# Optimization experiments

Hardware: AMD Instinct MI355X
Metric: run time of the kernel (lower is better)

Reference implementation:

```python
import jax, jax.numpy as jnp
import numpy as np

B = 64
SIZES = [5023, 1256, 314, 79, 20]
NV = [s + 1 for s in SIZES]          # vertex counts incl. padding vertex
K = 12                               # spiral length (all levels)
LAT = 128
ENC_F = [3, 16, 32, 64, 128]
DEC_IN = [128, 64, 32, 32, 16]
DEC_OUT = [64, 32, 32, 16, 3]


def setup_inputs() -> dict:
    keys = iter(jax.random.split(jax.random.key(0), 80))

    def nrm(shape, scale=1.0):
        return jax.random.normal(next(keys), shape, jnp.float32) * scale

    inp = {}
    inp['x_talking'] = nrm((B, NV[0], 3))
    inp['template'] = nrm((B, NV[0], 3))
    for i in range(4):
        inp['D%d' % i] = nrm((NV[i + 1], NV[i]), 1.0 / np.sqrt(NV[i]))
        inp['U%d' % i] = nrm((NV[i], NV[i + 1]), 1.0 / np.sqrt(NV[i + 1]))
    for i in range(4):
        fan = ENC_F[i] * K
        inp['enc_w%d' % i] = nrm((ENC_F[i + 1], fan), 1.0 / np.sqrt(fan))
        inp['enc_b%d' % i] = jnp.zeros((ENC_F[i + 1],), jnp.float32)
    inp['fc_enc_w'] = nrm((LAT, NV[4] * DEC_IN[0]), 1.0 / np.sqrt(NV[4] * DEC_IN[0]))
    inp['fc_enc_b'] = jnp.zeros((LAT,), jnp.float32)
    inp['fc_dec_w'] = nrm((NV[4] * DEC_IN[0], 2 * LAT), 1.0 / np.sqrt(2 * LAT))
    inp['fc_dec_b'] = jnp.zeros((NV[4] * DEC_IN[0],), jnp.float32)
    for i in range(5):
        fan = DEC_IN[i] * K
        inp['dec_w%d' % i] = nrm((DEC_OUT[i], fan), 1.0 / np.sqrt(fan))
        inp['dec_b%d' % i] = jnp.zeros((DEC_OUT[i],), jnp.float32)
    for i in range(4):
        inp['S%d' % i] = jax.random.randint(next(keys), (NV[i], K), 0, NV[i], jnp.int32)
    return inp


def _spiral_conv(x, S, W, b, act):
    # x: [B, N, F]; S: [N, K] spiral neighbor indices; W: [out, K*F] (torch Linear layout)
    Bv, Nv, F = x.shape
    g = x[:, S, :].reshape(Bv, Nv, K * F)            # spiral neighbor gather
    y = act(jnp.einsum('bnf,of->bno', g, W) + b)     # gather-GEMM + activation
    mask = jnp.ones((1, Nv, 1), y.dtype).at[0, -1, 0].set(0.0)  # zero out padding vertex
    return y * mask


def _forward(x_talking, template, D, U, enc, fc_enc_w, fc_enc_b, fc_dec_w, fc_dec_b, dec, S):
    elu = jax.nn.elu
    # encode_talking
    x = x_talking
    for i in range(4):
        x = _spiral_conv(x, S[i], enc[i][0], enc[i][1], elu)
        x = jnp.einsum('mn,bnf->bmf', D[i], x)       # downsample
    z = x.reshape(B, -1) @ fc_enc_w.T + fc_enc_b     # [B, latent]
    # decode(z, z)
    h = jnp.concatenate([z, z], axis=1) @ fc_dec_w.T + fc_dec_b
    x = h.reshape(B, NV[4], DEC_IN[0])
    for i in range(3):
        x = jnp.einsum('mn,bnf->bmf', U[3 - i], x)   # upsample
        x = _spiral_conv(x, S[3 - i], dec[i][0], dec[i][1], elu)
    x = jnp.einsum('mn,bnf->bmf', U[0], x)
    x = _spiral_conv(x, S[0], dec[3][0], dec[3][1], elu)
    x = _spiral_conv(x, S[0], dec[4][0], dec[4][1], lambda v: v)  # identity activation
    return x, x + template


def reference(x_talking, template, D0, D1, D2, D3, U0, U1, U2, U3,
              enc_w0, enc_b0, enc_w1, enc_b1, enc_w2, enc_b2, enc_w3, enc_b3,
              fc_enc_w, fc_enc_b, fc_dec_w, fc_dec_b,
              dec_w0, dec_b0, dec_w1, dec_b1, dec_w2, dec_b2, dec_w3, dec_b3, dec_w4, dec_b4,
              S0, S1, S2, S3):
    return _forward(
        x_talking, template,
        [D0, D1, D2, D3], [U0, U1, U2, U3],
        [(enc_w0, enc_b0), (enc_w1, enc_b1), (enc_w2, enc_b2), (enc_w3, enc_b3)],
        fc_enc_w, fc_enc_b, fc_dec_w, fc_dec_b,
        [(dec_w0, dec_b0), (dec_w1, dec_b1), (dec_w2, dec_b2), (dec_w3, dec_b3), (dec_w4, dec_b4)],
        [S0, S1, S2, S3])
```

## Files before the change

kernel.cpp:

```cpp
#include <hip/hip_runtime.h>
#include <cstddef>


#define BATCH 64
#define SPK 12

typedef __attribute__((ext_vector_type(8))) short bf16x8;
typedef __attribute__((ext_vector_type(4))) short bf16x4;
typedef __attribute__((ext_vector_type(4))) float f32x4;

__device__ __forceinline__ unsigned short f2bf(float x) {
    union { float f; unsigned int u; } v; v.f = x;
    unsigned int r = v.u + 0x7FFF + ((v.u >> 16) & 1);
    return (unsigned short)(r >> 16);
}

__global__ __launch_bounds__(256) void f32_to_bf16_kernel(
    const float* __restrict__ in, unsigned short* __restrict__ out, int n8)
{
    int i = blockIdx.x * 256 + threadIdx.x;
    if (i < n8) {
        const float* p = in + (size_t)i * 8;
        bf16x8 r;
#pragma unroll
        for (int j = 0; j < 8; ++j) r[j] = (short)f2bf(p[j]);
        *(bf16x8*)(out + (size_t)i * 8) = r;
    }
}

__global__ __launch_bounds__(256) void a_bf16_pad_kernel(
    const float* __restrict__ A, unsigned short* __restrict__ Ap,
    int M, int K, int Kp, int total)
{
    int i = blockIdx.x * 256 + threadIdx.x;
    if (i >= total) return;
    int kp8 = Kp >> 3;
    int m = i / kp8;
    int k0 = (i - m * kp8) * 8;
    bf16x8 r;
    if (m < M) {
        const float* src = A + (size_t)m * K + k0;
#pragma unroll
        for (int j = 0; j < 8; ++j) {
            float v = (k0 + j < K) ? src[j] : 0.f;
            r[j] = (short)f2bf(v);
        }
    } else {
#pragma unroll
        for (int j = 0; j < 8; ++j) r[j] = 0;
    }
    *(bf16x8*)(Ap + (size_t)m * Kp + k0) = r;
}

__global__ __launch_bounds__(256) void w_frag16_kernel(
    const unsigned short* __restrict__ Wb, unsigned short* __restrict__ Wfs,
    int KF, int total)
{
    int i = blockIdx.x * 256 + threadIdx.x;
    if (i >= total) return;
    int j    = i & 7;
    int lane = (i >> 3) & 63;
    int s    = i >> 9;
    int l15  = lane & 15;
    int quad = (lane >> 4) & 3;
    Wfs[i] = Wb[l15 * KF + s * 32 + quad * 8 + j];
}

template<int LOGF, int OBF16>
__global__ __launch_bounds__(64, 4) void conv_cmfma_kernel(
    const unsigned short* __restrict__ x, const int* __restrict__ S,
    const unsigned short* __restrict__ Wfs, const float* __restrict__ bias,
    void* __restrict__ yv, int Nv, int elu_flag, int swz)
{
    constexpr int F     = 1 << LOGF;
    constexpr int KF    = SPK * F;
    constexpr int NS    = KF / 32;
    constexpr int RPADu = (LOGF == 5) ? 40 : 24;
    __shared__ unsigned short Gs[12 * 16 * RPADu];

    const int lane = threadIdx.x;
    const int l15  = lane & 15;
    const int quad = (lane >> 4) & 3;

    int bx = blockIdx.x, bz = blockIdx.z;
    if (swz) {
        const int gx = gridDim.x;
        const int total = gx * gridDim.z;
        int bid = bx + gx * bz;
        const int chunk = total >> 3;
        int sid = (bid & 7) * chunk + (bid >> 3);
        bx = sid % gx;
        bz = sid / gx;
    }
    const int n0 = bx * 16;
    const int b  = bz;
    const size_t xb = (size_t)b * Nv;

    int4 sv;
    {
        int g = lane >> 4; if (g > 2) g = 2;
        int n = n0 + l15; if (n >= Nv) n = 0;
        sv = *(const int4*)(S + n * SPK + g * 4);
    }

    if constexpr (LOGF == 5) {
        const int grow = lane >> 2, gchk = lane & 3;
#pragma unroll
        for (int k = 0; k < 12; ++k) {
            int sel = ((k >> 2) << 4) | grow;
            int comp = k & 3;
            int src = (comp == 0) ? __shfl(sv.x, sel)
                    : (comp == 1) ? __shfl(sv.y, sel)
                    : (comp == 2) ? __shfl(sv.z, sel)
                                  : __shfl(sv.w, sel);
            bf16x8 v = *(const bf16x8*)(x + ((xb + src) << 5) + gchk * 8);
            *(bf16x8*)&Gs[k * 16 * RPADu + grow * RPADu + gchk * 8] = v;
        }
    } else {
        const int khalf = lane >> 5, grow = (lane >> 1) & 15, gchk = lane & 1;
#pragma unroll
        for (int g = 0; g < 6; ++g) {
            int k0 = 2 * g;
            int sel0 = ((k0 >> 2) << 4) | grow;
            int sel1 = (((k0 + 1) >> 2) << 4) | grow;
            int s0 = ((k0 & 3) == 0) ? __shfl(sv.x, sel0) : __shfl(sv.z, sel0);
            int s1 = (((k0 + 1) & 3) == 1) ? __shfl(sv.y, sel1) : __shfl(sv.w, sel1);
            int src = khalf ? s1 : s0;
            int k   = k0 + khalf;
            bf16x8 v = *(const bf16x8*)(x + ((xb + src) << 4) + gchk * 8);
            *(bf16x8*)&Gs[k * 16 * RPADu + grow * RPADu + gchk * 8] = v;
        }
    }

    f32x4 acc0 = (f32x4){0.f, 0.f, 0.f, 0.f};
    f32x4 acc1 = (f32x4){0.f, 0.f, 0.f, 0.f};
#pragma unroll
    for (int s = 0; s < NS; ++s) {
        int kf = s * 32 + quad * 8;
        int k  = kf >> LOGF;
        int f  = kf & (F - 1);
        bf16x8 a = *(const bf16x8*)&Gs[k * 16 * RPADu + l15 * RPADu + f];
        bf16x8 w = *(const bf16x8*)(Wfs + (s * 64 + lane) * 8);
        if (s & 1) acc1 = __builtin_amdgcn_mfma_f32_16x16x32_bf16(a, w, acc1, 0, 0, 0);
        else       acc0 = __builtin_amdgcn_mfma_f32_16x16x32_bf16(a, w, acc0, 0, 0, 0);
    }

    float bv = bias[l15];
#pragma unroll
    for (int reg = 0; reg < 4; ++reg) {
        int nn = n0 + quad * 4 + reg;
        if (nn >= Nv) continue;
        float v = acc0[reg] + acc1[reg] + bv;
        if (elu_flag && v <= 0.f) v = expm1f(v);
        if (nn == Nv - 1) v = 0.f;
        size_t off = ((size_t)b * Nv + nn) * 16 + l15;
        if (OBF16) ((unsigned short*)yv)[off] = f2bf(v);
        else       ((float*)yv)[off] = v;
    }
}

template<int LOGF, int OBF16>
__global__ __launch_bounds__(64) void conv_wmfma_kernel(
    const unsigned short* __restrict__ x, const int* __restrict__ S,
    const unsigned short* __restrict__ Wb, const float* __restrict__ bias,
    void* __restrict__ yv, int Nv, int O, int elu_flag, int swz)
{
    constexpr int F  = 1 << LOGF;
    constexpr int KF = SPK * F;
    constexpr int NS = KF / 32;
    const int lane = threadIdx.x;
    const int l15  = lane & 15;
    const int quad = lane >> 4;

    int bx = blockIdx.x, by = blockIdx.y, bz = blockIdx.z;
    if (swz) {
        const int gx = gridDim.x, gy = gridDim.y;
        const int total = gx * gy * gridDim.z;
        int bid = bx + gx * (by + gy * bz);
        const int chunk = total >> 3;
        int sid = (bid & 7) * chunk + (bid >> 3);
        bx = sid % gx; sid /= gx;
        by = sid % gy;
        bz = sid / gy;
    }

    const int n0   = bx * 16;
    const int o    = by * 16 + l15;
    const int b    = bz;
    const size_t xb = (size_t)b * Nv;

    const int n  = n0 + l15;
    const int ng = (n < Nv) ? n : 0;
    const unsigned short* wrow = Wb + (size_t)o * KF;

    f32x4 acc0 = (f32x4){0.f, 0.f, 0.f, 0.f};
    f32x4 acc1 = (f32x4){0.f, 0.f, 0.f, 0.f};
#pragma unroll
    for (int s = 0; s < NS; ++s) {
        int kf  = s * 32 + quad * 8;
        int k   = kf >> LOGF;
        int f   = kf & (F - 1);
        int src = S[ng * SPK + k];
        bf16x8 a = *(const bf16x8*)(x + ((xb + src) << LOGF) + f);
        bf16x8 w = *(const bf16x8*)(wrow + kf);
        if (s & 1) acc1 = __builtin_amdgcn_mfma_f32_16x16x32_bf16(a, w, acc1, 0, 0, 0);
        else       acc0 = __builtin_amdgcn_mfma_f32_16x16x32_bf16(a, w, acc0, 0, 0, 0);
    }
    float bv = bias[o];
#pragma unroll
    for (int reg = 0; reg < 4; ++reg) {
        int nn = n0 + quad * 4 + reg;
        if (nn >= Nv) continue;
        float v = acc0[reg] + acc1[reg] + bv;
        if (elu_flag && v <= 0.f) v = expm1f(v);
        if (nn == Nv - 1) v = 0.f;
        size_t off = ((size_t)b * Nv + nn) * O + o;
        if (OBF16) ((unsigned short*)yv)[off] = f2bf(v);
        else       ((float*)yv)[off] = v;
    }
}

template<int LOGF>
__global__ __launch_bounds__(256) void conv_mfma32_kernel(
    const unsigned short* __restrict__ x, const int* __restrict__ S,
    const unsigned short* __restrict__ Wb, const float* __restrict__ bias,
    float* __restrict__ y, int Nv, int KF, int elu_flag)
{
    constexpr int PAD = 40;
    __shared__ unsigned short Gs[2][256 * PAD];

    const int b    = blockIdx.x;
    const int n0   = blockIdx.y * 256;
    const int tid  = threadIdx.x;
    const int lane = tid & 63;
    const int wave = tid >> 6;
    const int wm   = wave * 64;
    const int l15  = lane & 15;
    const int quad = lane >> 4;
    const size_t xb = (size_t)b * Nv;
    const int nslab = KF >> 5;

    f32x4 acc[4][2];
#pragma unroll
    for (int t = 0; t < 4; ++t)
#pragma unroll
        for (int o = 0; o < 2; ++o) acc[t][o] = (f32x4){0.f, 0.f, 0.f, 0.f};

    auto gath = [&](int k0, bf16x8* g) {
        int n = n0 + tid;
        if (n < Nv) {
#pragma unroll
            for (int j = 0; j < 4; ++j) {
                int kf  = k0 + j * 8;
                int k   = kf >> LOGF;
                int f   = kf & ((1 << LOGF) - 1);
                int src = S[n * SPK + k];
                g[j] = *(const bf16x8*)(x + ((xb + src) << LOGF) + f);
            }
        } else {
#pragma unroll
            for (int j = 0; j < 4; ++j)
#pragma unroll
                for (int e = 0; e < 8; ++e) g[j][e] = 0;
        }
    };
    auto put = [&](int buf, const bf16x8* g) {
#pragma unroll
        for (int j = 0; j < 4; ++j)
            *(bf16x8*)&Gs[buf][tid * PAD + j * 8] = g[j];
    };
    auto wfrag = [&](int k0, int o16) {
        return *(const bf16x8*)(Wb + (size_t)(o16 * 16 + l15) * KF + k0 + quad * 8);
    };

    bf16x8 gcur[4], gnext[4];
    gath(0, gcur);
    put(0, gcur);
    __syncthreads();

    for (int s = 0; s < nslab; ++s) {
        const int cur = s & 1;
        const bool more = (s + 1) < nslab;
        if (more) gath((s + 1) * 32, gnext);
        bf16x8 wf0 = wfrag(s * 32, 0);
        bf16x8 wf1 = wfrag(s * 32, 1);
#pragma unroll
        for (int t = 0; t < 4; ++t) {
            bf16x8 a = *(const bf16x8*)&Gs[cur][(wm + t * 16 + l15) * PAD + quad * 8];
            acc[t][0] = __builtin_amdgcn_mfma_f32_16x16x32_bf16(a, wf0, acc[t][0], 0, 0, 0);
            acc[t][1] = __builtin_amdgcn_mfma_f32_16x16x32_bf16(a, wf1, acc[t][1], 0, 0, 0);
        }
        if (more) {
            put(cur ^ 1, gnext);
            __syncthreads();
        }
    }

    float bv0 = bias[l15];
    float bv1 = bias[16 + l15];
#pragma unroll
    for (int t = 0; t < 4; ++t)
#pragma unroll
        for (int reg = 0; reg < 4; ++reg) {
            int n = n0 + wm + t * 16 + quad * 4 + reg;
            if (n >= Nv) continue;
            float v0 = acc[t][0][reg] + bv0;
            float v1 = acc[t][1][reg] + bv1;
            if (elu_flag) {
                if (v0 <= 0.f) v0 = expm1f(v0);
                if (v1 <= 0.f) v1 = expm1f(v1);
            }
            if (n == Nv - 1) { v0 = 0.f; v1 = 0.f; }
            size_t off = ((size_t)b * Nv + n) * 32 + l15;
            y[off]      = v0;
            y[off + 16] = v1;
        }
}

__global__ __launch_bounds__(256) void dsamp_mfma3_kernel(
    const unsigned short* __restrict__ Ab, const unsigned short* __restrict__ Xt,
    float* __restrict__ Y, int M, int Kp, int logF, int kchunk,
    int atomic_flag, int swz)
{
    constexpr int PAD = 40;
    __shared__ unsigned short As[2][128 * PAD];
    __shared__ unsigned short Bs[2][128 * PAD];

    int bx = blockIdx.x, by = blockIdx.y, bz = blockIdx.z;
    if (swz) {
        const int gx = gridDim.x, gy = gridDim.y;
        const int total = gx * gy * gridDim.z;
        int bid = bx + gx * (by + gy * bz);
        const int chunk = total >> 3;
        int sid = (bid & 7) * chunk + (bid >> 3);
        bx = sid % gx; sid /= gx;
        by = sid % gy;
        bz = sid / gy;
    }

    const int fmask = (1 << logF) - 1;
    const int m0   = bx * 128;
    const int c0   = by * 128;
    const int kbeg = bz * kchunk;
    int kend = kbeg + kchunk; if (kend > Kp) kend = Kp;
    const int nslab = (kend - kbeg + 31) >> 5;

    const int tid  = threadIdx.x;
    const int lane = tid & 63;
    const int wave = tid >> 6;
    const int wm   = (wave >> 1) * 64;
    const int wn   = (wave & 1) * 64;
    const int l15  = lane & 15;
    const int quad = lane >> 4;

    const int s_row = tid >> 2;
    const int s_k8  = (tid & 3) * 8;

    f32x4 acc[4][4];
#pragma unroll
    for (int i = 0; i < 4; ++i)
#pragma unroll
        for (int j = 0; j < 4; ++j) acc[i][j] = (f32x4){0.f, 0.f, 0.f, 0.f};

    bf16x8 apre[2], bpre[2];

    auto loadAB = [&](int ko) {
        apre[0] = *(const bf16x8*)(Ab + (size_t)(m0 + s_row)      * Kp + ko + s_k8);
        apre[1] = *(const bf16x8*)(Ab + (size_t)(m0 + s_row + 64) * Kp + ko + s_k8);
        bpre[0] = *(const bf16x8*)(Xt + (size_t)(c0 + s_row)      * Kp + ko + s_k8);
        bpre[1] = *(const bf16x8*)(Xt + (size_t)(c0 + s_row + 64) * Kp + ko + s_k8);
    };
    auto stage = [&](int buf) {
        *(bf16x8*)&As[buf][s_row * PAD + s_k8]        = apre[0];
        *(bf16x8*)&As[buf][(s_row + 64) * PAD + s_k8] = apre[1];
        *(bf16x8*)&Bs[buf][s_row * PAD + s_k8]        = bpre[0];
        *(bf16x8*)&Bs[buf][(s_row + 64) * PAD + s_k8] = bpre[1];
    };

    loadAB(kbeg);
    stage(0);
    __syncthreads();

    for (int s = 0; s < nslab; ++s) {
        const int cur = s & 1;
        const bool more = (s + 1) < nslab;
        if (more) loadAB(kbeg + (s + 1) * 32);

        bf16x8 af[4], bfr[4];
#pragma unroll
        for (int t = 0; t < 4; ++t) {
            af[t]  = *(const bf16x8*)&As[cur][(wm + t * 16 + l15) * PAD + quad * 8];
            bfr[t] = *(const bf16x8*)&Bs[cur][(wn + t * 16 + l15) * PAD + quad * 8];
        }
#pragma unroll
        for (int tm = 0; tm < 4; ++tm)
#pragma unroll
            for (int tn = 0; tn < 4; ++tn)
                acc[tm][tn] = __builtin_amdgcn_mfma_f32_16x16x32_bf16(af[tm], bfr[tn], acc[tm][tn], 0, 0, 0);

        if (more) { stage(cur ^ 1); __syncthreads(); }
    }

#pragma unroll
    for (int tm = 0; tm < 4; ++tm)
#pragma unroll
        for (int tn = 0; tn < 4; ++tn)
#pragma unroll
            for (int reg = 0; reg < 4; ++reg) {
                int m  = m0 + wm + tm * 16 + quad * 4 + reg;
                int cc = c0 + wn + tn * 16 + l15;
                if (m < M) {
                    int bb = cc >> logF, f = cc & fmask;
                    float* dst = Y + (((size_t)bb * M + m) << logF) + f;
                    if (atomic_flag) atomicAdd(dst, acc[tm][tn][reg]);
                    else *dst = acc[tm][tn][reg];
                }
            }
}

__global__ __launch_bounds__(256) void dsamp_mfma2_kernel(
    const unsigned short* __restrict__ Ap, const float* __restrict__ X,
    float* __restrict__ Y, int M, int K, int Kp, int logF, int kchunk,
    int atomic_flag)
{
    constexpr int PAD = 40;
    __shared__ unsigned short Xs[2][64 * PAD];

    const int fmask = (1 << logF) - 1;
    const int m0   = blockIdx.x * 64;
    const int c0   = blockIdx.y * 64;
    const int kbeg = blockIdx.z * kchunk;
    int kend = kbeg + kchunk; if (kend > K) kend = K;
    const int nslab = (kend - kbeg + 31) >> 5;

    const int tid  = threadIdx.x;
    const int lane = tid & 63;
    const int wave = tid >> 6;
    const int wm   = (wave >> 1) * 32;
    const int wn   = (wave & 1) * 32;
    const int l15  = lane & 15;
    const int quad = lane >> 4;

    const int skk  = tid >> 4;
    const int scg  = (tid & 15) * 4;
    const int cB   = c0 + scg;
    const int xbb  = cB >> logF;
    const int xf   = cB & fmask;
    const size_t xrowbase = (((size_t)xbb * K) << logF) + xf;

    const int mA0 = m0 + wm + l15;
    const int mA1 = mA0 + 16;
    const int kaoff = quad * 8;

    f32x4 acc[2][2];
    acc[0][0] = acc[0][1] = acc[1][0] = acc[1][1] = (f32x4){0.f, 0.f, 0.f, 0.f};

    float4 xn0, xn1;
    bf16x8 ac0, ac1, an0, an1;

    {
        int k = kbeg + skk;
        xn0 = make_float4(0.f, 0.f, 0.f, 0.f);
        if (k < kend) xn0 = *(const float4*)(X + xrowbase + ((size_t)k << logF));
        k = kbeg + 16 + skk;
        xn1 = make_float4(0.f, 0.f, 0.f, 0.f);
        if (k < kend) xn1 = *(const float4*)(X + xrowbase + ((size_t)k << logF));
        int ka = kbeg + kaoff;
        ac0 = *(const bf16x8*)(Ap + (size_t)mA0 * Kp + ka);
        ac1 = *(const bf16x8*)(Ap + (size_t)mA1 * Kp + ka);
        unsigned short* p = &Xs[0][0];
        p[(scg + 0) * PAD + skk] = f2bf(xn0.x);
        p[(scg + 1) * PAD + skk] = f2bf(xn0.y);
        p[(scg + 2) * PAD + skk] = f2bf(xn0.z);
        p[(scg + 3) * PAD + skk] = f2bf(xn0.w);
        int kk1 = 16 + skk;
        p[(scg + 0) * PAD + kk1] = f2bf(xn1.x);
        p[(scg + 1) * PAD + kk1] = f2bf(xn1.y);
        p[(scg + 2) * PAD + kk1] = f2bf(xn1.z);
        p[(scg + 3) * PAD + kk1] = f2bf(xn1.w);
    }
    __syncthreads();

    for (int s = 0; s < nslab; ++s) {
        const int cur = s & 1;
        const bool more = (s + 1 < nslab);
        if (more) {
            int k0 = kbeg + (s + 1) * 32;
            int k = k0 + skk;
            xn0 = make_float4(0.f, 0.f, 0.f, 0.f);
            if (k < kend) xn0 = *(const float4*)(X + xrowbase + ((size_t)k << logF));
            k = k0 + 16 + skk;
            xn1 = make_float4(0.f, 0.f, 0.f, 0.f);
            if (k < kend) xn1 = *(const float4*)(X + xrowbase + ((size_t)k << logF));
            int ka = k0 + kaoff;
            an0 = *(const bf16x8*)(Ap + (size_t)mA0 * Kp + ka);
            an1 = *(const bf16x8*)(Ap + (size_t)mA1 * Kp + ka);
        }
        {
            const unsigned short* p = &Xs[cur][0];
            bf16x8 b0 = *(const bf16x8*)&p[(wn +      l15) * PAD + quad * 8];
            bf16x8 b1 = *(const bf16x8*)&p[(wn + 16 + l15) * PAD + quad * 8];
            acc[0][0] = __builtin_amdgcn_mfma_f32_16x16x32_bf16(ac0, b0, acc[0][0], 0, 0, 0);
            acc[0][1] = __builtin_amdgcn_mfma_f32_16x16x32_bf16(ac0, b1, acc[0][1], 0, 0, 0);
            acc[1][0] = __builtin_amdgcn_mfma_f32_16x16x32_bf16(ac1, b0, acc[1][0], 0, 0, 0);
            acc[1][1] = __builtin_amdgcn_mfma_f32_16x16x32_bf16(ac1, b1, acc[1][1], 0, 0, 0);
        }
        if (more) {
            unsigned short* q = &Xs[cur ^ 1][0];
            q[(scg + 0) * PAD + skk] = f2bf(xn0.x);
            q[(scg + 1) * PAD + skk] = f2bf(xn0.y);
            q[(scg + 2) * PAD + skk] = f2bf(xn0.z);
            q[(scg + 3) * PAD + skk] = f2bf(xn0.w);
            int kk1 = 16 + skk;
            q[(scg + 0) * PAD + kk1] = f2bf(xn1.x);
            q[(scg + 1) * PAD + kk1] = f2bf(xn1.y);
            q[(scg + 2) * PAD + kk1] = f2bf(xn1.z);
            q[(scg + 3) * PAD + kk1] = f2bf(xn1.w);
            __syncthreads();
            ac0 = an0; ac1 = an1;
        }
    }

#pragma unroll
    for (int tm = 0; tm < 2; ++tm)
#pragma unroll
        for (int tn = 0; tn < 2; ++tn)
#pragma unroll
            for (int reg = 0; reg < 4; ++reg) {
                int m  = m0 + wm + tm * 16 + quad * 4 + reg;
                int cc = c0 + wn + tn * 16 + l15;
                if (m < M) {
                    int bb = cc >> logF, f = cc & fmask;
                    float* dst = Y + (((size_t)bb * M + m) << logF) + f;
                    if (atomic_flag) atomicAdd(dst, acc[tm][tn][reg]);
                    else *dst = acc[tm][tn][reg];
                }
            }
}

template<int MT, int OT>
__global__ __launch_bounds__(256) void conv_gemm_kernel(
    const float* __restrict__ x, const int* __restrict__ S,
    const float* __restrict__ W, const float* __restrict__ bias,
    float* __restrict__ y, int Nv, int logF, int O, int KF, int KFr,
    int elu_flag)
{
    constexpr int CT = OT / 4;
    constexpr int RT = 256 / CT;
    static_assert(RT * 4 == MT, "tile shape");
    __shared__ float Gs[32][MT];
    __shared__ float Ws[32][OT];

    const int b   = blockIdx.x;
    const int n0  = blockIdx.y * MT;
    const int tid = threadIdx.x;
    const int cx  = tid % CT;
    const int ry  = tid / CT;
    const int r0  = ry * 4;
    const int o0  = cx * 4;
    const int fmask = (1 << logF) - 1;
    const size_t xb = (size_t)b * Nv;

    float acc[4][4];
#pragma unroll
    for (int i = 0; i < 4; ++i)
#pragma unroll
        for (int j = 0; j < 4; ++j) acc[i][j] = 0.f;

    for (int k0 = 0; k0 < KF; k0 += 32) {
        constexpr int GSLOTS = MT * 8;
#pragma unroll
        for (int i = 0; i < GSLOTS / 256; ++i) {
            int idx = tid + i * 256;
            int r   = idx & (MT - 1);
            int jg  = idx / MT;
            int j0  = jg * 4;
            int n   = n0 + r;
            int kf  = k0 + j0;
            float4 v = make_float4(0.f, 0.f, 0.f, 0.f);
            if (n < Nv && kf < KFr) {
                int k   = kf >> logF;
                int f   = kf & fmask;
                int src = S[n * SPK + k];
                v = *(const float4*)(x + ((xb + src) << logF) + f);
            }
            Gs[j0 + 0][r] = v.x; Gs[j0 + 1][r] = v.y;
            Gs[j0 + 2][r] = v.z; Gs[j0 + 3][r] = v.w;
        }
        constexpr int WSLOTS = OT * 8;
#pragma unroll
        for (int i = 0; i < (WSLOTS + 255) / 256; ++i) {
            int idx = tid + i * 256;
            if (WSLOTS >= 256 || idx < WSLOTS) {
                int o  = idx & (OT - 1);
                int jg = idx / OT;
                int j0 = jg * 4;
                float4 v = *(const float4*)(W + (size_t)o * KF + k0 + j0);
                Ws[j0 + 0][o] = v.x; Ws[j0 + 1][o] = v.y;
                Ws[j0 + 2][o] = v.z; Ws[j0 + 3][o] = v.w;
            }
        }
        __syncthreads();
#pragma unroll
        for (int kk = 0; kk < 32; ++kk) {
            float4 g = *(const float4*)&Gs[kk][r0];
            float4 w = *(const float4*)&Ws[kk][o0];
            acc[0][0] += g.x * w.x; acc[0][1] += g.x * w.y; acc[0][2] += g.x * w.z; acc[0][3] += g.x * w.w;
            acc[1][0] += g.y * w.x; acc[1][1] += g.y * w.y; acc[1][2] += g.y * w.z; acc[1][3] += g.y * w.w;
            acc[2][0] += g.z * w.x; acc[2][1] += g.z * w.y; acc[2][2] += g.z * w.z; acc[2][3] += g.z * w.w;
            acc[3][0] += g.w * w.x; acc[3][1] += g.w * w.y; acc[3][2] += g.w * w.z; acc[3][3] += g.w * w.w;
        }
        __syncthreads();
    }

    float4 bv = *(const float4*)(bias + o0);
#pragma unroll
    for (int i = 0; i < 4; ++i) {
        int n = n0 + r0 + i;
        if (n >= Nv) continue;
        float v0 = acc[i][0] + bv.x;
        float v1 = acc[i][1] + bv.y;
        float v2 = acc[i][2] + bv.z;
        float v3 = acc[i][3] + bv.w;
        if (elu_flag) {
            v0 = v0 > 0.f ? v0 : expm1f(v0);
            v1 = v1 > 0.f ? v1 : expm1f(v1);
            v2 = v2 > 0.f ? v2 : expm1f(v2);
            v3 = v3 > 0.f ? v3 : expm1f(v3);
        }
        if (n == Nv - 1) { v0 = v1 = v2 = v3 = 0.f; }
        *(float4*)(y + ((size_t)b * Nv + n) * O + o0) = make_float4(v0, v1, v2, v3);
    }
}

template<int OBF16>
__global__ __launch_bounds__(256) void dsamp_kernel(
    const float* __restrict__ A, const float* __restrict__ X,
    void* __restrict__ Yv, int M, int N, int F)
{
    __shared__ float As[16][68];
    __shared__ float Xs[16][64];

    const int m0  = blockIdx.x * 64;
    const int c0  = blockIdx.y * 64;
    const int tid = threadIdx.x;
    const int tx  = tid & 15;
    const int ty  = tid >> 4;

    float acc[4][4];
#pragma unroll
    for (int i = 0; i < 4; ++i)
#pragma unroll
        for (int j = 0; j < 4; ++j) acc[i][j] = 0.f;

    for (int k0 = 0; k0 < N; k0 += 16) {
#pragma unroll
        for (int p = 0; p < 4; ++p) {
            int r  = (tid >> 4) + p * 16;
            int kk = tid & 15;
            int m  = m0 + r;
            int n  = k0 + kk;
            float v = 0.f;
            if (m < M && n < N) v = A[(size_t)m * N + n];
            As[kk][r] = v;
        }
        {
            int kk = tid >> 4;
            int cc = (tid & 15) * 4;
            int n  = k0 + kk;
            float4 v = make_float4(0.f, 0.f, 0.f, 0.f);
            if (n < N) {
                int c  = c0 + cc;
                int bb = c / F;
                int f  = c - bb * F;
                v = *(const float4*)(X + ((size_t)bb * N + n) * F + f);
            }
            *(float4*)&Xs[kk][cc] = v;
        }
        __syncthreads();
#pragma unroll
        for (int kk = 0; kk < 16; ++kk) {
            float4 av = *(const float4*)&As[kk][ty * 4];
            float4 xv = *(const float4*)&Xs[kk][tx * 4];
            acc[0][0] += av.x * xv.x; acc[0][1] += av.x * xv.y; acc[0][2] += av.x * xv.z; acc[0][3] += av.x * xv.w;
            acc[1][0] += av.y * xv.x; acc[1][1] += av.y * xv.y; acc[1][2] += av.y * xv.z; acc[1][3] += av.y * xv.w;
            acc[2][0] += av.z * xv.x; acc[2][1] += av.z * xv.y; acc[2][2] += av.z * xv.z; acc[2][3] += av.z * xv.w;
            acc[3][0] += av.w * xv.x; acc[3][1] += av.w * xv.y; acc[3][2] += av.w * xv.z; acc[3][3] += av.w * xv.w;
        }
        __syncthreads();
    }

    const int cbase = c0 + tx * 4;
    const int bb = cbase / F;
    const int f  = cbase - bb * F;
#pragma unroll
    for (int i = 0; i < 4; ++i) {
        int m = m0 + ty * 4 + i;
        if (m < M) {
            size_t off = ((size_t)bb * M + m) * F + f;
            if (OBF16) {
                bf16x4 v;
                v[0] = (short)f2bf(acc[i][0]); v[1] = (short)f2bf(acc[i][1]);
                v[2] = (short)f2bf(acc[i][2]); v[3] = (short)f2bf(acc[i][3]);
                *(bf16x4*)((unsigned short*)Yv + off) = v;
            } else {
                *(float4*)((float*)Yv + off) =
                    make_float4(acc[i][0], acc[i][1], acc[i][2], acc[i][3]);
            }
        }
    }
}

__global__ __launch_bounds__(256) void fc_wave_kernel(
    const float* __restrict__ in, const float* __restrict__ W,
    const float* __restrict__ bias, float* __restrict__ out,
    int In, int O, int dup)
{
    const int gw   = blockIdx.x * 4 + (threadIdx.x >> 6);
    const int lane = threadIdx.x & 63;
    const int b = gw / O;
    const int o = gw - b * O;
    const float* xr = in + (size_t)b * In;
    float acc = 0.f;
    if (dup) {
        const float* wr = W + (size_t)o * (2 * In);
        for (int k = lane; k < In; k += 64)
            acc += xr[k] * (wr[k] + wr[In + k]);
    } else {
        const float* wr = W + (size_t)o * In;
        for (int k = lane; k < In; k += 64)
            acc += xr[k] * wr[k];
    }
#pragma unroll
    for (int off = 32; off > 0; off >>= 1)
        acc += __shfl_down(acc, off, 64);
    if (lane == 0) out[(size_t)b * O + o] = acc + bias[o];
}

__global__ __launch_bounds__(256) void xpose_bf16_kernel(
    const float* __restrict__ x, unsigned short* __restrict__ xt,
    int K, int Kp, int logF)
{
    const int c  = blockIdx.y * 256 + threadIdx.x;
    const int k0 = blockIdx.x * 8;
    const int bb = c >> logF;
    const int f  = c & ((1 << logF) - 1);
    const float* src = x + (((size_t)bb * K) << logF) + f;
    bf16x8 r;
#pragma unroll
    for (int j = 0; j < 8; ++j) {
        int k = k0 + j;
        float v = (k < K) ? src[(size_t)k << logF] : 0.f;
        r[j] = (short)f2bf(v);
    }
    *(bf16x8*)(xt + (size_t)c * Kp + k0) = r;
}

__global__ __launch_bounds__(256) void pad_e0_w_kernel(
    const float* __restrict__ w, float* __restrict__ wp)
{
    int i = blockIdx.x * 256 + threadIdx.x;
    if (i < 1024) {
        int o = i >> 6, kf = i & 63;
        int k = kf >> 2, f = kf & 3;
        wp[i] = (f < 3 && k < 12) ? w[o * 36 + k * 3 + f] : 0.f;
    }
}
__global__ __launch_bounds__(256) void pad_x4_kernel(
    const float* __restrict__ x, float* __restrict__ xp, int n)
{
    int i = blockIdx.x * 256 + threadIdx.x;
    if (i < n) {
        int f = i & 3, nb = i >> 2;
        xp[i] = (f < 3) ? x[nb * 3 + f] : 0.f;
    }
}
__global__ __launch_bounds__(256) void pad_c4_w_kernel(
    const float* __restrict__ w, const float* __restrict__ b,
    float* __restrict__ wp, float* __restrict__ bp)
{
    int i = blockIdx.x * 256 + threadIdx.x;
    if (i < 3072) {
        int o = i / 192;
        wp[i] = (o < 3) ? w[i] : 0.f;
    }
    if (i < 16) bp[i] = (i < 3) ? b[i] : 0.f;
}
__global__ __launch_bounds__(256) void extract_add_kernel(
    const float* __restrict__ cp, const float* __restrict__ t,
    float* __restrict__ o0, float* __restrict__ o1, int n)
{
    int i = blockIdx.x * 256 + threadIdx.x;
    if (i < n) {
        int f = i % 3, nb = i / 3;
        float v = cp[(size_t)nb * 16 + f];
        o0[i] = v;
        o1[i] = v + t[i];
    }
}


static inline int ilog2(int v) { int l = 0; while ((1 << l) < v) ++l; return l; }

static inline void a_bf16_launch(const float* A, unsigned short* Ap, int M, int K,
                                 int Mp, int Kp, hipStream_t s)
{
    int total = Mp * (Kp >> 3);
    a_bf16_pad_kernel<<<(total + 255) / 256, 256, 0, s>>>(A, Ap, M, K, Kp, total);
}

static inline void dsamp_mfma2_launch(const unsigned short* Ap, const float* X,
                                      float* Y, int M, int K, int Kp, int F,
                                      int ks, hipStream_t s)
{
    int kchunk = (K + ks - 1) / ks;
    kchunk = (kchunk + 31) & ~31;
    int ksz = (K + kchunk - 1) / kchunk;
    dim3 grid((M + 63) / 64, F, ksz);
    dsamp_mfma2_kernel<<<grid, 256, 0, s>>>(Ap, X, Y, M, K, Kp, ilog2(F), kchunk,
                                            ksz > 1 ? 1 : 0);
}

static inline void dsamp_mfma3_launch(const unsigned short* Ab, const unsigned short* Xt,
                                      float* Y, int M, int Kp, int F,
                                      int ks, hipStream_t s)
{
    int slabs = Kp >> 5;
    int kchunk = ((slabs + ks - 1) / ks) * 32;
    int ksz = (Kp + kchunk - 1) / kchunk;
    int gx = (M + 127) / 128, gy = (BATCH * F) / 128;
    int total = gx * gy * ksz;
    int swz = (ksz > 1 && (total & 7) == 0) ? 1 : 0;
    dim3 grid(gx, gy, ksz);
    dsamp_mfma3_kernel<<<grid, 256, 0, s>>>(Ab, Xt, Y, M, Kp, ilog2(F), kchunk,
                                            ksz > 1 ? 1 : 0, swz);
}

template<int OBF16>
static inline void dsamp_launch(const float* A, const float* X, void* Y,
                                int M, int N, int F, hipStream_t s)
{
    dim3 grid((M + 63) / 64, F);
    dsamp_kernel<OBF16><<<grid, 256, 0, s>>>(A, X, Y, M, N, F);
}

extern "C" void kernel_launch(void* const* d_in, const int* in_sizes, int n_in,
                              void* d_out, int out_size, void* d_ws, size_t ws_size,
                              hipStream_t stream)
{
    const float* x_talking = (const float*)d_in[0];
    const float* templ     = (const float*)d_in[1];
    const float* D0 = (const float*)d_in[2];
    const float* U0 = (const float*)d_in[3];
    const float* D1 = (const float*)d_in[4];
    const float* U1 = (const float*)d_in[5];
    const float* D2 = (const float*)d_in[6];
    const float* U2 = (const float*)d_in[7];
    const float* D3 = (const float*)d_in[8];
    const float* U3 = (const float*)d_in[9];
    const float* enc_w0 = (const float*)d_in[10]; const float* enc_b0 = (const float*)d_in[11];
    const float* enc_w1 = (const float*)d_in[12]; const float* enc_b1 = (const float*)d_in[13];
    const float* enc_w2 = (const float*)d_in[14]; const float* enc_b2 = (const float*)d_in[15];
    const float* enc_w3 = (const float*)d_in[16]; const float* enc_b3 = (const float*)d_in[17];
    const float* fc_enc_w = (const float*)d_in[18]; const float* fc_enc_b = (const float*)d_in[19];
    const float* fc_dec_w = (const float*)d_in[20]; const float* fc_dec_b = (const float*)d_in[21];
    const float* dec_w0 = (const float*)d_in[22]; const float* dec_b0 = (const float*)d_in[23];
    const float* dec_w1 = (const float*)d_in[24]; const float* dec_b1 = (const float*)d_in[25];
    const float* dec_w2 = (const float*)d_in[26]; const float* dec_b2 = (const float*)d_in[27];
    const float* dec_w3 = (const float*)d_in[28]; const float* dec_b3 = (const float*)d_in[29];
    const float* dec_w4 = (const float*)d_in[30]; const float* dec_b4 = (const float*)d_in[31];
    const int* S0 = (const int*)d_in[32];
    const int* S1 = (const int*)d_in[33];
    const int* S2 = (const int*)d_in[34];
    const int* S3 = (const int*)d_in[35];

    float* bufA = (float*)d_ws;
    float* bufB = bufA + 10289152;

    float* out0 = (float*)d_out;
    float* out1 = out0 + 964608;

    unsigned short* Xt_e0 = (unsigned short*)(bufB + 1290240);
    unsigned short* Xt_c2 = (unsigned short*)bufB;
    unsigned short* U0b   = (unsigned short*)(bufB + 1400000);
    unsigned short* Wb_e2 = (unsigned short*)(bufB + 4700000);
    unsigned short* Wb_e3 = (unsigned short*)(bufB + 4715000);
    unsigned short* Wb_c0 = (unsigned short*)(bufB + 4765000);
    unsigned short* Wb_c1 = (unsigned short*)(bufB + 4815000);
    float* xpad   = bufA + 5200000;
    float* WpE0   = bufA + 6600000;
    unsigned short* D0b   = (unsigned short*)(bufA + 6700000);
    unsigned short* D1b   = (unsigned short*)(bufA + 9950000);
    unsigned short* U1b   = (unsigned short*)(bufA + 4000000);
    unsigned short* Wb_e1 = (unsigned short*)(bufA + 10160000);
    unsigned short* Wb_c2 = (unsigned short*)(bufA + 10170000);
    unsigned short* Xb_e1   = (unsigned short*)(bufA + 5200000);
    unsigned short* Xb_e2   = (unsigned short*)(bufA + 2000000);
    unsigned short* Xb_c2in = (unsigned short*)(bufA + 2600000);
    unsigned short* Xb_c3 = (unsigned short*)bufB;
    unsigned short* Xb_c4 = (unsigned short*)(bufA + 5200000);
    unsigned short* Wb_c3 = (unsigned short*)bufA;
    float* WpC4   = bufA + 10000;
    float* BpC4   = bufA + 13500;
    unsigned short* Wb_c4  = (unsigned short*)(bufA + 14000);
    unsigned short* Wfs_c3 = (unsigned short*)(bufA + 16000);
    unsigned short* Wfs_c4 = (unsigned short*)(bufA + 20000);

    hipMemsetAsync(bufB, 0, (size_t)1287168 * sizeof(float), stream);

    pad_e0_w_kernel<<<4, 256, 0, stream>>>(enc_w0, WpE0);
    pad_x4_kernel<<<5024, 256, 0, stream>>>(x_talking, xpad, 1286144);
    a_bf16_launch(D0, D0b, 1257, 5024, 1280, 5024, stream);
    a_bf16_launch(D1, D1b, 315, 1257, 320, 1280, stream);
    f32_to_bf16_kernel<<<3, 256, 0, stream>>>(enc_w1, Wb_e1, 768);
    f32_to_bf16_kernel<<<6, 256, 0, stream>>>(dec_w2, Wb_c2, 1536);
    f32_to_bf16_kernel<<<12, 256, 0, stream>>>(enc_w2, Wb_e2, 3072);
    f32_to_bf16_kernel<<<48, 256, 0, stream>>>(enc_w3, Wb_e3, 12288);
    f32_to_bf16_kernel<<<48, 256, 0, stream>>>(dec_w0, Wb_c0, 12288);
    f32_to_bf16_kernel<<<12, 256, 0, stream>>>(dec_w1, Wb_c1, 3072);

    {
        dim3 grid(BATCH, (5024 + 255) / 256);
        conv_gemm_kernel<256, 16><<<grid, 256, 0, stream>>>(
            xpad, S0, WpE0, enc_b0, bufA, 5024, 2, 16, 64, 48, 1);
    }
    xpose_bf16_kernel<<<dim3(628, 4), 256, 0, stream>>>(bufA, Xt_e0, 5024, 5024, 4);
    dsamp_mfma3_launch(D0b, Xt_e0, bufB, 1257, 5024, 16, 8, stream);
    f32_to_bf16_kernel<<<629, 256, 0, stream>>>(bufB, Xb_e1, 160896);
    a_bf16_launch(U0, U0b, 5024, 1257, 5120, 1280, stream);
    a_bf16_launch(U1, U1b, 1257, 315, 1280, 320, stream);
    {
        dim3 grid(BATCH, (1257 + 255) / 256);
        conv_mfma32_kernel<4><<<grid, 256, 0, stream>>>(
            Xb_e1, S1, Wb_e1, enc_b1, bufA, 1257, 192, 1);
    }
    hipMemsetAsync(bufB, 0, (size_t)645120 * sizeof(float), stream);
    dsamp_mfma2_launch(D1b, bufA, bufB, 315, 1257, 1280, 32, 8, stream);
    f32_to_bf16_kernel<<<315, 256, 0, stream>>>(bufB, Xb_e2, 80640);
    {
        dim3 grid((315 + 15) / 16, 64 / 16, BATCH);
        conv_wmfma_kernel<5, 0><<<grid, 64, 0, stream>>>(
            Xb_e2, S2, Wb_e2, enc_b2, bufA, 315, 64, 1, 0);
    }
    dsamp_launch<1>(D2, bufA, bufB, 80, 315, 64, stream);
    {
        dim3 grid((80 + 15) / 16, 128 / 16, BATCH);
        conv_wmfma_kernel<6, 0><<<grid, 64, 0, stream>>>(
            (const unsigned short*)bufB, S3, Wb_e3, enc_b3, bufA, 80, 128, 1, 0);
    }
    dsamp_launch<0>(D3, bufA, bufB, 21, 80, 128, stream);

    fc_wave_kernel<<<dim3((BATCH * 128) / 4), 256, 0, stream>>>(bufB, fc_enc_w, fc_enc_b, bufA, 2688, 128, 0);
    fc_wave_kernel<<<dim3((BATCH * 2688) / 4), 256, 0, stream>>>(bufA, fc_dec_w, fc_dec_b, bufB, 128, 2688, 1);

    dsamp_launch<1>(U3, bufB, bufA, 80, 21, 128, stream);
    {
        dim3 grid((80 + 15) / 16, 64 / 16, BATCH);
        conv_wmfma_kernel<7, 0><<<grid, 64, 0, stream>>>(
            (const unsigned short*)bufA, S3, Wb_c0, dec_b0, bufB, 80, 64, 1, 0);
    }
    dsamp_launch<1>(U2, bufB, bufA, 315, 80, 64, stream);
    {
        dim3 grid((315 + 15) / 16, 32 / 16, BATCH);
        conv_wmfma_kernel<6, 0><<<grid, 64, 0, stream>>>(
            (const unsigned short*)bufA, S2, Wb_c1, dec_b1, bufB, 315, 32, 1, 0);
    }
    dsamp_mfma2_launch(U1b, bufB, bufA, 1257, 315, 320, 32, 1, stream);
    f32_to_bf16_kernel<<<1257, 256, 0, stream>>>(bufA, Xb_c2in, 321792);
    {
        dim3 grid(BATCH, (1257 + 255) / 256);
        conv_mfma32_kernel<5><<<grid, 256, 0, stream>>>(
            Xb_c2in, S1, Wb_c2, dec_b2, bufA, 1257, 384, 1);
    }
    xpose_bf16_kernel<<<dim3(160, 8), 256, 0, stream>>>(bufA, Xt_c2, 1257, 1280, 5);
    dsamp_mfma3_launch(U0b, Xt_c2, bufA, 5024, 1280, 32, 1, stream);

    f32_to_bf16_kernel<<<5024, 256, 0, stream>>>(bufA, Xb_c3, 1286144);
    f32_to_bf16_kernel<<<3, 256, 0, stream>>>(dec_w3, Wb_c3, 768);
    w_frag16_kernel<<<24, 256, 0, stream>>>(Wb_c3, Wfs_c3, 384, 6144);
    pad_c4_w_kernel<<<12, 256, 0, stream>>>(dec_w4, dec_b4, WpC4, BpC4);
    f32_to_bf16_kernel<<<2, 256, 0, stream>>>(WpC4, Wb_c4, 384);
    w_frag16_kernel<<<12, 256, 0, stream>>>(Wb_c4, Wfs_c4, 192, 3072);
    {
        dim3 grid(5024 / 16, 1, BATCH);
        conv_cmfma_kernel<5, 1><<<grid, 64, 0, stream>>>(
            Xb_c3, S0, Wfs_c3, dec_b3, (void*)Xb_c4, 5024, 1, 1);
    }
    {
        dim3 grid(5024 / 16, 1, BATCH);
        conv_cmfma_kernel<4, 0><<<grid, 64, 0, stream>>>(
            Xb_c4, S0, Wfs_c4, BpC4, (void*)bufB, 5024, 0, 1);
    }
    extract_add_kernel<<<(964608 + 255) / 256, 256, 0, stream>>>(bufB, templ, out0, out1, 964608);
}
```

Measured before the change: 717.0 us.

## Replace split-K atomics with partial buffers and fuse bf16 output conversion

The split-K downsample GEMMs now write per-split partial sums to separate buffers instead of using atomicAdd into memset-cleared outputs. A new kernel sums the four partials and converts to bf16 in one pass, which removes the memsets and the separate f32-to-bf16 conversion launches. The upsample GEMMs without split-K now write bf16 directly from the epilogue, and the split count drops from 8 to 4. This costs extra partial-buffer traffic and needs the buffer layout reshuffled, so overlapping regions are a risk.

After: 671.7 us. 6.3% less time.

```diff
diff --git a/kernel.cpp b/kernel.cpp
--- a/kernel.cpp
+++ b/kernel.cpp
@@ -25,6 +25,24 @@
 #pragma unroll
         for (int j = 0; j < 8; ++j) r[j] = (short)f2bf(p[j]);
         *(bf16x8*)(out + (size_t)i * 8) = r;
+    }
+}
+
+__global__ __launch_bounds__(256) void reduce4_bf16_kernel(
+    const float* __restrict__ P, size_t ps, unsigned short* __restrict__ out,
+    int n8)
+{
+    int i = blockIdx.x * 256 + threadIdx.x;
+    if (i < n8) {
+        size_t base = (size_t)i * 8;
+        bf16x8 r;
+#pragma unroll
+        for (int j = 0; j < 8; ++j) {
+            float v = P[base + j] + P[ps + base + j]
+                    + P[2 * ps + base + j] + P[3 * ps + base + j];
+            r[j] = (short)f2bf(v);
+        }
+        *(bf16x8*)(out + base) = r;
     }
 }
 
@@ -317,10 +335,11 @@
         }
 }
 
+template<int OBF16>
 __global__ __launch_bounds__(256) void dsamp_mfma3_kernel(
     const unsigned short* __restrict__ Ab, const unsigned short* __restrict__ Xt,
-    float* __restrict__ Y, int M, int Kp, int logF, int kchunk,
-    int atomic_flag, int swz)
+    void* __restrict__ Yv, int M, int Kp, int logF, int kchunk,
+    int atomic_flag, int swz, size_t pstride)
 {
     constexpr int PAD = 40;
     __shared__ unsigned short As[2][128 * PAD];
@@ -344,6 +363,7 @@
     const int kbeg = bz * kchunk;
     int kend = kbeg + kchunk; if (kend > Kp) kend = Kp;
     const int nslab = (kend - kbeg + 31) >> 5;
+    const size_t zoff = (size_t)bz * pstride;
 
     const int tid  = threadIdx.x;
     const int lane = tid & 63;
@@ -411,17 +431,20 @@
                 int cc = c0 + wn + tn * 16 + l15;
                 if (m < M) {
                     int bb = cc >> logF, f = cc & fmask;
-                    float* dst = Y + (((size_t)bb * M + m) << logF) + f;
-                    if (atomic_flag) atomicAdd(dst, acc[tm][tn][reg]);
-                    else *dst = acc[tm][tn][reg];
+                    size_t off = zoff + (((size_t)bb * M + m) << logF) + f;
+                    float v = acc[tm][tn][reg];
+                    if (OBF16)            ((unsigned short*)Yv)[off] = f2bf(v);
+                    else if (atomic_flag) atomicAdd((float*)Yv + off, v);
+                    else                  ((float*)Yv)[off] = v;
                 }
             }
 }
 
+template<int OBF16>
 __global__ __launch_bounds__(256) void dsamp_mfma2_kernel(
     const unsigned short* __restrict__ Ap, const float* __restrict__ X,
-    float* __restrict__ Y, int M, int K, int Kp, int logF, int kchunk,
-    int atomic_flag)
+    void* __restrict__ Yv, int M, int K, int Kp, int logF, int kchunk,
+    int atomic_flag, size_t pstride)
 {
     constexpr int PAD = 40;
     __shared__ unsigned short Xs[2][64 * PAD];
@@ -432,6 +455,7 @@
     const int kbeg = blockIdx.z * kchunk;
     int kend = kbeg + kchunk; if (kend > K) kend = K;
     const int nslab = (kend - kbeg + 31) >> 5;
+    const size_t zoff = (size_t)blockIdx.z * pstride;
 
     const int tid  = threadIdx.x;
     const int lane = tid & 63;
@@ -531,9 +555,11 @@
                 int cc = c0 + wn + tn * 16 + l15;
                 if (m < M) {
                     int bb = cc >> logF, f = cc & fmask;
-                    float* dst = Y + (((size_t)bb * M + m) << logF) + f;
-                    if (atomic_flag) atomicAdd(dst, acc[tm][tn][reg]);
-                    else *dst = acc[tm][tn][reg];
+                    size_t off = zoff + (((size_t)bb * M + m) << logF) + f;
+                    float v = acc[tm][tn][reg];
+                    if (OBF16)            ((unsigned short*)Yv)[off] = f2bf(v);
+                    else if (atomic_flag) atomicAdd((float*)Yv + off, v);
+                    else                  ((float*)Yv)[off] = v;
                 }
             }
 }
@@ -809,31 +835,37 @@
     a_bf16_pad_kernel<<<(total + 255) / 256, 256, 0, s>>>(A, Ap, M, K, Kp, total);
 }
 
+template<int OBF16>
 static inline void dsamp_mfma2_launch(const unsigned short* Ap, const float* X,
-                                      float* Y, int M, int K, int Kp, int F,
-                                      int ks, hipStream_t s)
+                                      void* Y, int M, int K, int Kp, int F,
+                                      int ks, int partial, hipStream_t s)
 {
     int kchunk = (K + ks - 1) / ks;
     kchunk = (kchunk + 31) & ~31;
     int ksz = (K + kchunk - 1) / kchunk;
+    int atomic = (ksz > 1 && !partial) ? 1 : 0;
+    size_t pstride = (partial && ksz > 1) ? (size_t)BATCH * M * F : 0;
     dim3 grid((M + 63) / 64, F, ksz);
-    dsamp_mfma2_kernel<<<grid, 256, 0, s>>>(Ap, X, Y, M, K, Kp, ilog2(F), kchunk,
-                                            ksz > 1 ? 1 : 0);
-}
-
+    dsamp_mfma2_kernel<OBF16><<<grid, 256, 0, s>>>(Ap, X, Y, M, K, Kp, ilog2(F),
+                                                   kchunk, atomic, pstride);
+}
+
+template<int OBF16>
 static inline void dsamp_mfma3_launch(const unsigned short* Ab, const unsigned short* Xt,
-                                      float* Y, int M, int Kp, int F,
-                                      int ks, hipStream_t s)
+                                      void* Y, int M, int Kp, int F,
+                                      int ks, int partial, hipStream_t s)
 {
     int slabs = Kp >> 5;
     int kchunk = ((slabs + ks - 1) / ks) * 32;
     int ksz = (Kp + kchunk - 1) / kchunk;
     int gx = (M + 127) / 128, gy = (BATCH * F) / 128;
     int total = gx * gy * ksz;
-    int swz = (ksz > 1 && (total & 7) == 0) ? 1 : 0;
+    int swz = ((total & 7) == 0) ? 1 : 0;
+    int atomic = (ksz > 1 && !partial) ? 1 : 0;
+    size_t pstride = (partial && ksz > 1) ? (size_t)BATCH * M * F : 0;
     dim3 grid(gx, gy, ksz);
-    dsamp_mfma3_kernel<<<grid, 256, 0, s>>>(Ab, Xt, Y, M, Kp, ilog2(F), kchunk,
-                                            ksz > 1 ? 1 : 0, swz);
+    dsamp_mfma3_kernel<OBF16><<<grid, 256, 0, s>>>(Ab, Xt, Y, M, Kp, ilog2(F),
+                                                   kchunk, atomic, swz, pstride);
 }
 
 template<int OBF16>
@@ -894,19 +926,19 @@
     unsigned short* U1b   = (unsigned short*)(bufA + 4000000);
     unsigned short* Wb_e1 = (unsigned short*)(bufA + 10160000);
     unsigned short* Wb_c2 = (unsigned short*)(bufA + 10170000);
-    unsigned short* Xb_e1   = (unsigned short*)(bufA + 5200000);
+    float*          Pd0   = bufA;
+    unsigned short* Xb_e1 = (unsigned short*)(bufA + 5200000);
+    float*          Pd1   = bufA + 5200000;
     unsigned short* Xb_e2   = (unsigned short*)(bufA + 2000000);
     unsigned short* Xb_c2in = (unsigned short*)(bufA + 2600000);
-    unsigned short* Xb_c3 = (unsigned short*)bufB;
-    unsigned short* Xb_c4 = (unsigned short*)(bufA + 5200000);
-    unsigned short* Wb_c3 = (unsigned short*)bufA;
-    float* WpC4   = bufA + 10000;
-    float* BpC4   = bufA + 13500;
-    unsigned short* Wb_c4  = (unsigned short*)(bufA + 14000);
-    unsigned short* Wfs_c3 = (unsigned short*)(bufA + 16000);
-    unsigned short* Wfs_c4 = (unsigned short*)(bufA + 20000);
-
-    hipMemsetAsync(bufB, 0, (size_t)1287168 * sizeof(float), stream);
+    unsigned short* Xb_c3n  = (unsigned short*)bufA;
+    unsigned short* Xb_c4   = (unsigned short*)(bufA + 5200000);
+    unsigned short* Wb_c3  = (unsigned short*)(bufA + 7800000);
+    unsigned short* Wfs_c3 = (unsigned short*)(bufA + 7805000);
+    float* WpC4   = bufA + 7810000;
+    float* BpC4   = bufA + 7813500;
+    unsigned short* Wb_c4  = (unsigned short*)(bufA + 7814000);
+    unsigned short* Wfs_c4 = (unsigned short*)(bufA + 7818000);
 
     pad_e0_w_kernel<<<4, 256, 0, stream>>>(enc_w0, WpE0);
     pad_x4_kernel<<<5024, 256, 0, stream>>>(x_talking, xpad, 1286144);
@@ -925,8 +957,8 @@
             xpad, S0, WpE0, enc_b0, bufA, 5024, 2, 16, 64, 48, 1);
     }
     xpose_bf16_kernel<<<dim3(628, 4), 256, 0, stream>>>(bufA, Xt_e0, 5024, 5024, 4);
-    dsamp_mfma3_launch(D0b, Xt_e0, bufB, 1257, 5024, 16, 8, stream);
-    f32_to_bf16_kernel<<<629, 256, 0, stream>>>(bufB, Xb_e1, 160896);
+    dsamp_mfma3_launch<0>(D0b, Xt_e0, Pd0, 1257, 5024, 16, 4, 1, stream);
+    reduce4_bf16_kernel<<<629, 256, 0, stream>>>(Pd0, 1287168, Xb_e1, 160896);
     a_bf16_launch(U0, U0b, 5024, 1257, 5120, 1280, stream);
     a_bf16_launch(U1, U1b, 1257, 315, 1280, 320, stream);
     {
@@ -934,9 +966,8 @@
         conv_mfma32_kernel<4><<<grid, 256, 0, stream>>>(
             Xb_e1, S1, Wb_e1, enc_b1, bufA, 1257, 192, 1);
     }
-    hipMemsetAsync(bufB, 0, (size_t)645120 * sizeof(float), stream);
-    dsamp_mfma2_launch(D1b, bufA, bufB, 315, 1257, 1280, 32, 8, stream);
-    f32_to_bf16_kernel<<<315, 256, 0, stream>>>(bufB, Xb_e2, 80640);
+    dsamp_mfma2_launch<0>(D1b, bufA, Pd1, 315, 1257, 1280, 32, 4, 1, stream);
+    reduce4_bf16_kernel<<<315, 256, 0, stream>>>(Pd1, 645120, Xb_e2, 80640);
     {
         dim3 grid((315 + 15) / 16, 64 / 16, BATCH);
         conv_wmfma_kernel<5, 0><<<grid, 64, 0, stream>>>(
@@ -965,17 +996,15 @@
         conv_wmfma_kernel<6, 0><<<grid, 64, 0, stream>>>(
             (const unsigned short*)bufA, S2, Wb_c1, dec_b1, bufB, 315, 32, 1, 0);
     }
-    dsamp_mfma2_launch(U1b, bufB, bufA, 1257, 315, 320, 32, 1, stream);
-    f32_to_bf16_kernel<<<1257, 256, 0, stream>>>(bufA, Xb_c2in, 321792);
+    dsamp_mfma2_launch<1>(U1b, bufB, Xb_c2in, 1257, 315, 320, 32, 1, 0, stream);
     {
         dim3 grid(BATCH, (1257 + 255) / 256);
         conv_mfma32_kernel<5><<<grid, 256, 0, stream>>>(
             Xb_c2in, S1, Wb_c2, dec_b2, bufA, 1257, 384, 1);
     }
     xpose_bf16_kernel<<<dim3(160, 8), 256, 0, stream>>>(bufA, Xt_c2, 1257, 1280, 5);
-    dsamp_mfma3_launch(U0b, Xt_c2, bufA, 5024, 1280, 32, 1, stream);
-
-    f32_to_bf16_kernel<<<5024, 256, 0, stream>>>(bufA, Xb_c3, 1286144);
+    dsamp_mfma3_launch<1>(U0b, Xt_c2, Xb_c3n, 5024, 1280, 32, 1, 0, stream);
+
     f32_to_bf16_kernel<<<3, 256, 0, stream>>>(dec_w3, Wb_c3, 768);
     w_frag16_kernel<<<24, 256, 0, stream>>>(Wb_c3, Wfs_c3, 384, 6144);
     pad_c4_w_kernel<<<12, 256, 0, stream>>>(dec_w4, dec_b4, WpC4, BpC4);
@@ -984,7 +1013,7 @@
     {
         dim3 grid(5024 / 16, 1, BATCH);
         conv_cmfma_kernel<5, 1><<<grid, 64, 0, stream>>>(
-            Xb_c3, S0, Wfs_c3, dec_b3, (void*)Xb_c4, 5024, 1, 1);
+            Xb_c3n, S0, Wfs_c3, dec_b3, (void*)Xb_c4, 5024, 1, 1);
     }
     {
         dim3 grid(5024 / 16, 1, BATCH);
```
